# Kernel tuning notes

Measured on AMD Instinct MI355X. Metric: run time of the kernel, lower is better.

## Reference

```python
import jax, jax.numpy as jnp
import numpy as np

MARGIN = 0.3


def setup_inputs() -> dict:
    key = jax.random.key(0)
    k1, k2 = jax.random.split(key)
    N, D = 8192, 128
    embeddings = jax.random.normal(k1, (N, D), dtype=jnp.float32)
    labels = jax.random.randint(k2, (N,), 0, 512, dtype=jnp.int64)
    return {"embeddings": embeddings, "labels": labels}


def _pairwise_dist(x):
    # Euclidean cdist via squared-norm expansion; safe sqrt (zero grad at d==0).
    sq_norms = jnp.sum(x * x, axis=-1)  # [N]
    sq = sq_norms[:, None] + sq_norms[None, :] - 2.0 * (x @ x.T)  # [N, N]
    sq = jnp.maximum(sq, 0.0)
    safe = jnp.where(sq > 0.0, sq, 1.0)
    return jnp.where(sq > 0.0, jnp.sqrt(safe), 0.0)


def reference(embeddings, labels):
    d = _pairwise_dist(embeddings)  # [N, N]
    same = labels[:, None] == labels[None, :]
    eye = jnp.eye(labels.shape[0], dtype=bool)
    pos_mask = same & ~eye
    neg_mask = ~same

    inf = jnp.float32(jnp.inf)
    hardest_pos = jnp.max(jnp.where(pos_mask, d, -inf), axis=1)  # [N]
    hardest_neg = jnp.min(jnp.where(neg_mask, d, inf), axis=1)   # [N]

    valid = jnp.any(pos_mask, axis=1) & jnp.any(neg_mask, axis=1)
    per_row = jax.nn.relu(hardest_pos - hardest_neg + MARGIN)
    per_row = jnp.where(valid, per_row, 0.0)
    count = jnp.sum(valid)
    return jnp.where(count > 0, jnp.sum(per_row) / jnp.maximum(count, 1), 0.0)
```

## Files before the change

### kernel.cpp

```cpp
#include <hip/hip_runtime.h>
#include <hip/hip_fp16.h>

#define N 8192
#define D 128
#define MARGIN 0.3f

typedef __fp16 half_t;
typedef __attribute__((ext_vector_type(8))) __fp16 half8;
typedef __attribute__((ext_vector_type(4))) float f32x4;

__global__ void triplet_prep(const float* __restrict__ x,
                             half_t* __restrict__ xp,
                             float* __restrict__ norms,
                             float* __restrict__ gacc) {
    __shared__ float wpart[4][16];
    const int b   = blockIdx.x;
    const int i   = threadIdx.x;
    if (b == 0 && i < 3) gacc[i] = 0.f;
    const int row = b * 16 + (i & 15);
    const int kb  = i >> 4;
    const float* rp = x + (size_t)row * D + kb * 8;
    float v[8];
#pragma unroll
    for (int e = 0; e < 8; ++e) v[e] = rp[e];
    half_t h[8];
#pragma unroll
    for (int e = 0; e < 8; ++e) h[e] = (half_t)v[e];
    *(half8*)(xp + ((size_t)b * 256 + i) * 8) = *(const half8*)h;

    float s = 0.f;
#pragma unroll
    for (int e = 0; e < 8; ++e) s = fmaf(v[e], v[e], s);
    s += __shfl_xor(s, 16);
    s += __shfl_xor(s, 32);
    const int w = i >> 6, lane = i & 63;
    if (lane < 16) wpart[w][lane] = s;
    __syncthreads();
    if (i < 16) norms[row - (i & 15) + i] =
        wpart[0][i] + wpart[1][i] + wpart[2][i] + wpart[3][i];
}


#define PF(BN, LJN, NJN, SN) {                                          \
    const half_t* bp = xp + ((size_t)(colbase >> 4) + (SN)) * 2048 + lane * 8; \
    BN[0] = *(const half8*)bp;                                          \
    BN[1] = *(const half8*)(bp + 512);                                  \
    BN[2] = *(const half8*)(bp + 1024);                                 \
    BN[3] = *(const half8*)(bp + 1536);                                 \
    const int jn = colbase + (SN) * 16 + lcol;                          \
    LJN = labels[jn];                                                   \
    NJN = norms[jn];                                                    \
}

#define POISON(ACC) {                                                   \
    _Pragma("unroll")                                                   \
    for (int rg = 0; rg < 4; ++rg)                                      \
        ACC[rg] = (diagl && rg == drg) ? -1e30f : ACC[rg];              \
}

#define EPI(ACC, FI, LJC) {                                             \
    _Pragma("unroll")                                                   \
    for (int rg = 0; rg < 4; ++rg) {                                    \
        float c = ACC[rg];                                              \
        bool same = (li[(FI) * 4 + rg] == (LJC));                       \
        mpos[(FI)*4+rg] = same ? fmaxf(mpos[(FI)*4+rg], c) : mpos[(FI)*4+rg]; \
        mneg[(FI)*4+rg] = same ? mneg[(FI)*4+rg] : fminf(mneg[(FI)*4+rg], c); \
    }                                                                   \
}

#define COMP(BC, LJC, NJC, S) {                                         \
    f32x4 njq = {NJC, NJC, NJC, NJC};                                   \
    __builtin_amdgcn_s_setprio(1);                                      \
    f32x4 a0 = __builtin_amdgcn_mfma_f32_16x16x32_f16(af[0][0], BC[0], njq, 0, 0, 0); \
    f32x4 a1 = __builtin_amdgcn_mfma_f32_16x16x32_f16(af[1][0], BC[0], njq, 0, 0, 0); \
    f32x4 a2 = __builtin_amdgcn_mfma_f32_16x16x32_f16(af[2][0], BC[0], njq, 0, 0, 0); \
    f32x4 a3 = __builtin_amdgcn_mfma_f32_16x16x32_f16(af[3][0], BC[0], njq, 0, 0, 0); \
    _Pragma("unroll")                                                   \
    for (int ks = 1; ks < 4; ++ks) {                                    \
        a0 = __builtin_amdgcn_mfma_f32_16x16x32_f16(af[0][ks], BC[ks], a0, 0, 0, 0); \
        a1 = __builtin_amdgcn_mfma_f32_16x16x32_f16(af[1][ks], BC[ks], a1, 0, 0, 0); \
        a2 = __builtin_amdgcn_mfma_f32_16x16x32_f16(af[2][ks], BC[ks], a2, 0, 0, 0); \
        a3 = __builtin_amdgcn_mfma_f32_16x16x32_f16(af[3][ks], BC[ks], a3, 0, 0, 0); \
    }                                                                   \
    __builtin_amdgcn_s_setprio(0);                                      \
    const int dj = colbase + (S) * 16 - rowbase;                        \
    if (dj == 0)       POISON(a0)                                       \
    else if (dj == 16) POISON(a1)                                       \
    else if (dj == 32) POISON(a2)                                       \
    else if (dj == 48) POISON(a3)                                       \
    EPI(a0, 0, LJC)                                                     \
    EPI(a1, 1, LJC)                                                     \
    EPI(a2, 2, LJC)                                                     \
    EPI(a3, 3, LJC)                                                     \
}

__launch_bounds__(512)
__global__ void triplet_main(const half_t* __restrict__ xp,
                             const float* __restrict__ norms,
                             const int* __restrict__ labels,
                             float* __restrict__ ppos,
                             float* __restrict__ pneg) {
    const int tid   = threadIdx.x;
    const int lane  = tid & 63;
    const int b     = blockIdx.x;
    const int chunk = b & 31;
    const int rowg  = (b >> 5) * 8 + (tid >> 6);
    const int lrow  = lane >> 4;
    const int lcol  = lane & 15;
    const int rowbase = rowg * 64;
    const int colbase = chunk * 256;
    const bool diagl = (lrow == (lcol >> 2));
    const int  drg   = lcol & 3;

    half8 af[4][4];
#pragma unroll
    for (int fi = 0; fi < 4; ++fi) {
        const half_t* ap = xp + ((size_t)(rowbase >> 4) + fi) * 2048 + lane * 8;
#pragma unroll
        for (int ks = 0; ks < 4; ++ks)
            af[fi][ks] = *(const half8*)(ap + ks * 512) * (half_t)(-2.0f);
    }

    const int ibase = rowbase + lrow * 4;
    int li[16];
#pragma unroll
    for (int fi = 0; fi < 4; ++fi)
#pragma unroll
        for (int rg = 0; rg < 4; ++rg)
            li[fi * 4 + rg] = labels[ibase + fi * 16 + rg];

    float mpos[16], mneg[16];
#pragma unroll
    for (int r = 0; r < 16; ++r) { mpos[r] = -1e38f; mneg[r] = 1e38f; }

    half8 b0[4], b1[4], b2[4];
    int lj0, lj1, lj2; float nj0, nj1, nj2;
    PF(b0, lj0, nj0, 0)
    PF(b1, lj1, nj1, 1)
    for (int s = 0; s < 12; s += 3) {
        PF(b2, lj2, nj2, s + 2)
        COMP(b0, lj0, nj0, s)
        PF(b0, lj0, nj0, s + 3)
        COMP(b1, lj1, nj1, s + 1)
        PF(b1, lj1, nj1, s + 4)
        COMP(b2, lj2, nj2, s + 2)
    }
    PF(b2, lj2, nj2, 14)
    COMP(b0, lj0, nj0, 12)
    PF(b0, lj0, nj0, 15)
    COMP(b1, lj1, nj1, 13)
    COMP(b2, lj2, nj2, 14)
    COMP(b0, lj0, nj0, 15)

#pragma unroll
    for (int o = 1; o < 16; o <<= 1) {
#pragma unroll
        for (int r = 0; r < 16; ++r) {
            mpos[r] = fmaxf(mpos[r], __shfl_xor(mpos[r], o));
            mneg[r] = fminf(mneg[r], __shfl_xor(mneg[r], o));
        }
    }
    if (lcol == 0) {
#pragma unroll
        for (int fi = 0; fi < 4; ++fi)
#pragma unroll
            for (int rg = 0; rg < 4; ++rg) {
                int row = ibase + fi * 16 + rg;
                ppos[(size_t)row * 32 + chunk] = mpos[fi * 4 + rg];
                pneg[(size_t)row * 32 + chunk] = mneg[fi * 4 + rg];
            }
    }
}

__global__ void triplet_reduce(const float* __restrict__ ppos,
                               const float* __restrict__ pneg,
                               const float* __restrict__ norms,
                               float* __restrict__ gacc,
                               float* __restrict__ out) {
    __shared__ float ss[256];
    __shared__ float sc[256];
    const int tid = threadIdx.x;
    const int r   = blockIdx.x * 256 + tid;
    float mp = -1e38f, mn = 1e38f;
    const f32x4* pp = (const f32x4*)(ppos + (size_t)r * 32);
    const f32x4* pn = (const f32x4*)(pneg + (size_t)r * 32);
#pragma unroll
    for (int s4 = 0; s4 < 8; ++s4) {
        f32x4 a = pp[s4], b = pn[s4];
#pragma unroll
        for (int e = 0; e < 4; ++e) { mp = fmaxf(mp, a[e]); mn = fminf(mn, b[e]); }
    }
    float ni = norms[r];
    bool valid = (mp > -1e37f) && (mn < 1e37f);
    float hp = sqrtf(fmaxf(ni + mp, 0.f));
    float hn = sqrtf(fmaxf(ni + mn, 0.f));
    float pr = fmaxf(hp - hn + MARGIN, 0.f);
    ss[tid] = valid ? pr : 0.f;
    sc[tid] = valid ? 1.f : 0.f;
    __syncthreads();
    for (int o = 128; o > 0; o >>= 1) {
        if (tid < o) { ss[tid] += ss[tid + o]; sc[tid] += sc[tid + o]; }
        __syncthreads();
    }
    if (tid == 0) {
        atomicAdd(&gacc[0], ss[0]);
        atomicAdd(&gacc[1], sc[0]);
        __threadfence();
        unsigned* ticket = (unsigned*)(gacc + 2);
        unsigned old = atomicAdd(ticket, 1u);
        if (old == gridDim.x - 1) {
            float s = atomicAdd(&gacc[0], 0.f);
            float c = atomicAdd(&gacc[1], 0.f);
            out[0] = (c > 0.f) ? (s / c) : 0.f;
        }
    }
}

extern "C" void kernel_launch(void* const* d_in, const int* in_sizes, int n_in,
                              void* d_out, int out_size, void* d_ws, size_t ws_size,
                              hipStream_t stream) {
    const float* x      = (const float*)d_in[0];
    const int*   labels = (const int*)d_in[1];
    float*       out    = (float*)d_out;

    char*   ws    = (char*)d_ws;
    half_t* xp    = (half_t*)ws;
    float*  norms = (float*)(ws + (size_t)N * D * sizeof(half_t));
    float*  ppos  = norms + N;
    float*  pneg  = ppos + (size_t)N * 32;
    float*  gacc  = pneg + (size_t)N * 32;

    triplet_prep  <<<N / 16,   256, 0, stream>>>(x, xp, norms, gacc);
    triplet_main  <<<512,      512, 0, stream>>>(xp, norms, labels, ppos, pneg);
    triplet_reduce<<<N / 256,  256, 0, stream>>>(ppos, pneg, norms, gacc, out);
}
```

Baseline: 51.86 us.

## Stage column tiles in LDS via direct global-to-LDS loads with double buffering

The main kernel now loads each 16-column B tile once per block into shared memory using global_load_lds with a two-stage buffer, instead of every wave loading it separately from global memory into registers. Labels and norms are packed into a float2 array in the prep kernel, so one LDS staging load supplies both. This cuts redundant global/L2 traffic across the 8 waves of a block. In exchange it adds a block-wide barrier and a full vmcnt wait every tile, which may serialise the loads with compute.

New measurement: 93.23 us. 79.8% more time.

```diff
diff --git a/kernel.cpp b/kernel.cpp
--- a/kernel.cpp
+++ b/kernel.cpp
@@ -9,9 +9,13 @@
 typedef __attribute__((ext_vector_type(8))) __fp16 half8;
 typedef __attribute__((ext_vector_type(4))) float f32x4;
 
+#define AS1C(p) ((const __attribute__((address_space(1))) void*)(p))
+#define AS3(p)  ((__attribute__((address_space(3))) void*)(p))
+
 __global__ void triplet_prep(const float* __restrict__ x,
+                             const int* __restrict__ labels,
                              half_t* __restrict__ xp,
-                             float* __restrict__ norms,
+                             float2* __restrict__ lnj,
                              float* __restrict__ gacc) {
     __shared__ float wpart[4][16];
     const int b   = blockIdx.x;
@@ -36,21 +40,14 @@
     const int w = i >> 6, lane = i & 63;
     if (lane < 16) wpart[w][lane] = s;
     __syncthreads();
-    if (i < 16) norms[row - (i & 15) + i] =
-        wpart[0][i] + wpart[1][i] + wpart[2][i] + wpart[3][i];
-}
-
-
-#define PF(BN, LJN, NJN, SN) {                                          \
-    const half_t* bp = xp + ((size_t)(colbase >> 4) + (SN)) * 2048 + lane * 8; \
-    BN[0] = *(const half8*)bp;                                          \
-    BN[1] = *(const half8*)(bp + 512);                                  \
-    BN[2] = *(const half8*)(bp + 1024);                                 \
-    BN[3] = *(const half8*)(bp + 1536);                                 \
-    const int jn = colbase + (SN) * 16 + lcol;                          \
-    LJN = labels[jn];                                                   \
-    NJN = norms[jn];                                                    \
-}
+    if (i < 16) {
+        const int r = b * 16 + i;
+        float nv = wpart[0][i] + wpart[1][i] + wpart[2][i] + wpart[3][i];
+        float2 p; p.x = __int_as_float(labels[r]); p.y = nv;
+        lnj[r] = p;
+    }
+}
+
 
 #define POISON(ACC) {                                                   \
     _Pragma("unroll")                                                   \
@@ -68,38 +65,15 @@
     }                                                                   \
 }
 
-#define COMP(BC, LJC, NJC, S) {                                         \
-    f32x4 njq = {NJC, NJC, NJC, NJC};                                   \
-    __builtin_amdgcn_s_setprio(1);                                      \
-    f32x4 a0 = __builtin_amdgcn_mfma_f32_16x16x32_f16(af[0][0], BC[0], njq, 0, 0, 0); \
-    f32x4 a1 = __builtin_amdgcn_mfma_f32_16x16x32_f16(af[1][0], BC[0], njq, 0, 0, 0); \
-    f32x4 a2 = __builtin_amdgcn_mfma_f32_16x16x32_f16(af[2][0], BC[0], njq, 0, 0, 0); \
-    f32x4 a3 = __builtin_amdgcn_mfma_f32_16x16x32_f16(af[3][0], BC[0], njq, 0, 0, 0); \
-    _Pragma("unroll")                                                   \
-    for (int ks = 1; ks < 4; ++ks) {                                    \
-        a0 = __builtin_amdgcn_mfma_f32_16x16x32_f16(af[0][ks], BC[ks], a0, 0, 0, 0); \
-        a1 = __builtin_amdgcn_mfma_f32_16x16x32_f16(af[1][ks], BC[ks], a1, 0, 0, 0); \
-        a2 = __builtin_amdgcn_mfma_f32_16x16x32_f16(af[2][ks], BC[ks], a2, 0, 0, 0); \
-        a3 = __builtin_amdgcn_mfma_f32_16x16x32_f16(af[3][ks], BC[ks], a3, 0, 0, 0); \
-    }                                                                   \
-    __builtin_amdgcn_s_setprio(0);                                      \
-    const int dj = colbase + (S) * 16 - rowbase;                        \
-    if (dj == 0)       POISON(a0)                                       \
-    else if (dj == 16) POISON(a1)                                       \
-    else if (dj == 32) POISON(a2)                                       \
-    else if (dj == 48) POISON(a3)                                       \
-    EPI(a0, 0, LJC)                                                     \
-    EPI(a1, 1, LJC)                                                     \
-    EPI(a2, 2, LJC)                                                     \
-    EPI(a3, 3, LJC)                                                     \
-}
-
 __launch_bounds__(512)
 __global__ void triplet_main(const half_t* __restrict__ xp,
-                             const float* __restrict__ norms,
+                             const float2* __restrict__ lnjg,
                              const int* __restrict__ labels,
                              float* __restrict__ ppos,
                              float* __restrict__ pneg) {
+    __shared__ __align__(16) half_t Bs[2][2048];
+    __shared__ __align__(16) float2 Lns[256];
+
     const int tid   = threadIdx.x;
     const int lane  = tid & 63;
     const int b     = blockIdx.x;
@@ -112,6 +86,17 @@
     const bool diagl = (lrow == (lcol >> 2));
     const int  drg   = lcol & 3;
 
+    if (tid < 256)
+        __builtin_amdgcn_global_load_lds(
+            AS1C(xp + (size_t)(colbase >> 4) * 2048 + tid * 8),
+            AS3(&Bs[0][tid * 8]), 16, 0, 0);
+    else if (tid < 384) {
+        const int i = tid - 256;
+        __builtin_amdgcn_global_load_lds(
+            AS1C((const char*)(lnjg + colbase) + i * 16),
+            AS3((char*)&Lns[0] + i * 16), 16, 0, 0);
+    }
+
     half8 af[4][4];
 #pragma unroll
     for (int fi = 0; fi < 4; ++fi) {
@@ -133,24 +118,60 @@
 #pragma unroll
     for (int r = 0; r < 16; ++r) { mpos[r] = -1e38f; mneg[r] = 1e38f; }
 
-    half8 b0[4], b1[4], b2[4];
-    int lj0, lj1, lj2; float nj0, nj1, nj2;
-    PF(b0, lj0, nj0, 0)
-    PF(b1, lj1, nj1, 1)
-    for (int s = 0; s < 12; s += 3) {
-        PF(b2, lj2, nj2, s + 2)
-        COMP(b0, lj0, nj0, s)
-        PF(b0, lj0, nj0, s + 3)
-        COMP(b1, lj1, nj1, s + 1)
-        PF(b1, lj1, nj1, s + 4)
-        COMP(b2, lj2, nj2, s + 2)
-    }
-    PF(b2, lj2, nj2, 14)
-    COMP(b0, lj0, nj0, 12)
-    PF(b0, lj0, nj0, 15)
-    COMP(b1, lj1, nj1, 13)
-    COMP(b2, lj2, nj2, 14)
-    COMP(b0, lj0, nj0, 15)
+    asm volatile("s_waitcnt vmcnt(0)" ::: "memory");
+    __builtin_amdgcn_s_barrier();
+    __builtin_amdgcn_sched_barrier(0);
+
+#pragma unroll
+    for (int t = 0; t < 16; ++t) {
+        if (t < 15 && tid < 256)
+            __builtin_amdgcn_global_load_lds(
+                AS1C(xp + ((size_t)(colbase >> 4) + t + 1) * 2048 + tid * 8),
+                AS3(&Bs[(t + 1) & 1][tid * 8]), 16, 0, 0);
+
+        const half_t* bp = &Bs[t & 1][lane * 8];
+        half8 bv0 = *(const half8*)bp;
+        half8 bv1 = *(const half8*)(bp + 512);
+        half8 bv2 = *(const half8*)(bp + 1024);
+        half8 bv3 = *(const half8*)(bp + 1536);
+        float2 p = Lns[t * 16 + lcol];
+        const int   lj = __float_as_int(p.x);
+        const float nj = p.y;
+
+        f32x4 njq = {nj, nj, nj, nj};
+        __builtin_amdgcn_s_setprio(1);
+        f32x4 a0 = __builtin_amdgcn_mfma_f32_16x16x32_f16(af[0][0], bv0, njq, 0, 0, 0);
+        f32x4 a1 = __builtin_amdgcn_mfma_f32_16x16x32_f16(af[1][0], bv0, njq, 0, 0, 0);
+        f32x4 a2 = __builtin_amdgcn_mfma_f32_16x16x32_f16(af[2][0], bv0, njq, 0, 0, 0);
+        f32x4 a3 = __builtin_amdgcn_mfma_f32_16x16x32_f16(af[3][0], bv0, njq, 0, 0, 0);
+        a0 = __builtin_amdgcn_mfma_f32_16x16x32_f16(af[0][1], bv1, a0, 0, 0, 0);
+        a1 = __builtin_amdgcn_mfma_f32_16x16x32_f16(af[1][1], bv1, a1, 0, 0, 0);
+        a2 = __builtin_amdgcn_mfma_f32_16x16x32_f16(af[2][1], bv1, a2, 0, 0, 0);
+        a3 = __builtin_amdgcn_mfma_f32_16x16x32_f16(af[3][1], bv1, a3, 0, 0, 0);
+        a0 = __builtin_amdgcn_mfma_f32_16x16x32_f16(af[0][2], bv2, a0, 0, 0, 0);
+        a1 = __builtin_amdgcn_mfma_f32_16x16x32_f16(af[1][2], bv2, a1, 0, 0, 0);
+        a2 = __builtin_amdgcn_mfma_f32_16x16x32_f16(af[2][2], bv2, a2, 0, 0, 0);
+        a3 = __builtin_amdgcn_mfma_f32_16x16x32_f16(af[3][2], bv2, a3, 0, 0, 0);
+        a0 = __builtin_amdgcn_mfma_f32_16x16x32_f16(af[0][3], bv3, a0, 0, 0, 0);
+        a1 = __builtin_amdgcn_mfma_f32_16x16x32_f16(af[1][3], bv3, a1, 0, 0, 0);
+        a2 = __builtin_amdgcn_mfma_f32_16x16x32_f16(af[2][3], bv3, a2, 0, 0, 0);
+        a3 = __builtin_amdgcn_mfma_f32_16x16x32_f16(af[3][3], bv3, a3, 0, 0, 0);
+        __builtin_amdgcn_s_setprio(0);
+
+        const int dj = colbase + t * 16 - rowbase;
+        if (dj == 0)       POISON(a0)
+        else if (dj == 16) POISON(a1)
+        else if (dj == 32) POISON(a2)
+        else if (dj == 48) POISON(a3)
+        EPI(a0, 0, lj)
+        EPI(a1, 1, lj)
+        EPI(a2, 2, lj)
+        EPI(a3, 3, lj)
+
+        asm volatile("s_waitcnt vmcnt(0)" ::: "memory");
+        __builtin_amdgcn_s_barrier();
+        __builtin_amdgcn_sched_barrier(0);
+    }
 
 #pragma unroll
     for (int o = 1; o < 16; o <<= 1) {
@@ -174,7 +195,7 @@
 
 __global__ void triplet_reduce(const float* __restrict__ ppos,
                                const float* __restrict__ pneg,
-                               const float* __restrict__ norms,
+                               const float2* __restrict__ lnjg,
                                float* __restrict__ gacc,
                                float* __restrict__ out) {
     __shared__ float ss[256];
@@ -190,7 +211,7 @@
 #pragma unroll
         for (int e = 0; e < 4; ++e) { mp = fmaxf(mp, a[e]); mn = fminf(mn, b[e]); }
     }
-    float ni = norms[r];
+    float ni = lnjg[r].y;
     bool valid = (mp > -1e37f) && (mn < 1e37f);
     float hp = sqrtf(fmaxf(ni + mp, 0.f));
     float hn = sqrtf(fmaxf(ni + mn, 0.f));
@@ -225,12 +246,12 @@
 
     char*   ws    = (char*)d_ws;
     half_t* xp    = (half_t*)ws;
-    float*  norms = (float*)(ws + (size_t)N * D * sizeof(half_t));
-    float*  ppos  = norms + N;
+    float2* lnj   = (float2*)(ws + (size_t)N * D * sizeof(half_t));
+    float*  ppos  = (float*)(lnj + N);
     float*  pneg  = ppos + (size_t)N * 32;
     float*  gacc  = pneg + (size_t)N * 32;
 
-    triplet_prep  <<<N / 16,   256, 0, stream>>>(x, xp, norms, gacc);
-    triplet_main  <<<512,      512, 0, stream>>>(xp, norms, labels, ppos, pneg);
-    triplet_reduce<<<N / 256,  256, 0, stream>>>(ppos, pneg, norms, gacc, out);
-}
+    triplet_prep  <<<N / 16,   256, 0, stream>>>(x, labels, xp, lnj, gacc);
+    triplet_main  <<<512,      512, 0, stream>>>(xp, lnj, labels, ppos, pneg);
+    triplet_reduce<<<N / 256,  256, 0, stream>>>(ppos, pneg, lnj, gacc, out);
+}
```
